# Optimization experiments

Measured on AMD Instinct MI355X. Metric: run time of the kernel, lower is better.

Reference implementation:

```python
import jax, jax.numpy as jnp
import numpy as np

B, C, H, W = 16, 512, 48, 48
INTER = 64  # C // reduction


def setup_inputs() -> dict:
    key = jax.random.key(0)
    k1, k2, k3, k4, k5 = jax.random.split(key, 5)
    s = 0.05
    return {
        "x": jax.random.normal(k1, (B, C, H, W), dtype=jnp.float32),
        "Wq": jax.random.normal(k2, (INTER, C), dtype=jnp.float32) * s,
        "Wk": jax.random.normal(k3, (INTER, C), dtype=jnp.float32) * s,
        "Wv": jax.random.normal(k4, (C, C), dtype=jnp.float32) * s,
        "gamma": jax.random.normal(k5, (1,), dtype=jnp.float32),
    }


def reference(x, Wq, Wk, Wv, gamma):
    b, c, h, w = x.shape
    n = h * w
    xf = x.reshape(b, c, n)                       # (B, C, N)
    # 1x1 convs == channel-mixing GEMMs
    q = jnp.einsum("ic,bcn->bin", Wq, xf)         # (B, inter, N)
    k = jnp.einsum("ic,bcn->bin", Wk, xf)         # (B, inter, N)
    v = jnp.einsum("oc,bcn->bon", Wv, xf)         # (B, C, N)
    # attn[b, n, m] = q[b, :, n] . k[b, :, m]; softmax over m
    attn = jnp.einsum("bin,bim->bnm", q, k)       # (B, N, N)
    attn = jax.nn.softmax(attn, axis=-1)
    # out[b, c, n] = sum_m v[b, c, m] * attn[b, n, m]
    out = jnp.einsum("bcm,bnm->bcn", v, attn).reshape(b, c, h, w)
    return gamma[0] * out + x
```

## Files before the change

kernel.cpp:

```cpp
#include <hip/hip_runtime.h>

#define BATCH 16
#define CHN   512
#define INTER 64
#define NPIX  2304

typedef _Float16 f16;
typedef _Float16 f16x8 __attribute__((ext_vector_type(8)));
typedef _Float16 f16x4 __attribute__((ext_vector_type(4)));
typedef short    s16x8 __attribute__((ext_vector_type(8)));
typedef float    f32x16 __attribute__((ext_vector_type(16)));

#define XT_OFF   ((size_t)0)
#define QT_OFF   ((size_t)37748736)
#define KT_OFF   ((size_t)42467328)
#define VB_OFF   ((size_t)47185920)
#define WHQ_OFF  ((size_t)84934656)
#define WHK_OFF  ((size_t)85000192)
#define WHV_OFF  ((size_t)85065728)

#define LOG2E 1.4426950408889634f

__device__ inline unsigned short f2bf(float f) {
    unsigned int u = __float_as_uint(f);
    unsigned int r = (u + 0x7FFFu + ((u >> 16) & 1u)) >> 16;
    return (unsigned short)r;
}

__device__ inline unsigned pack_bf16(float a, float b) {
    unsigned ua = __float_as_uint(a) + 0x8000u;
    unsigned ub = __float_as_uint(b) + 0x8000u;
    return __builtin_amdgcn_perm(ub, ua, 0x07060302u);
}

__device__ inline unsigned pack_f16(float a, float b) {
    f16 ha = (f16)a, hb = (f16)b;
    unsigned short ua = *(unsigned short*)&ha, ub = *(unsigned short*)&hb;
    return (unsigned)ua | ((unsigned)ub << 16);
}

__device__ inline float exp2_fast(float x) {
#if __has_builtin(__builtin_amdgcn_exp2f)
    return __builtin_amdgcn_exp2f(x);
#else
    float r; asm("v_exp_f32 %0, %1" : "=v"(r) : "v"(x)); return r;
#endif
}

__device__ inline void gload_lds16(const void* g, void* l) {
    __builtin_amdgcn_global_load_lds(
        (const __attribute__((address_space(1))) void*)g,
        (__attribute__((address_space(3))) void*)l, 16, 0, 0);
}

__device__ inline void swap32(unsigned x, unsigned y, unsigned& nx, unsigned& ny, int lh) {
#if __has_builtin(__builtin_amdgcn_permlane32_swap)
    auto r = __builtin_amdgcn_permlane32_swap(x, y, false, false);
    nx = r[0]; ny = r[1];
#else
    const unsigned xs = (unsigned)__shfl_xor((int)x, 32, 64);
    const unsigned ys = (unsigned)__shfl_xor((int)y, 32, 64);
    nx = lh ? ys : x;
    ny = lh ? y  : xs;
#endif
}

__global__ __launch_bounds__(256) void convert_x_kernel(
    const float* __restrict__ x, f16* __restrict__ xT)
{
    const int n0 = blockIdx.x * 64;
    const int c0 = blockIdx.y * 64;
    const int b  = blockIdx.z;
    const int t  = threadIdx.x;

    __shared__ float tile[64][65];

    {
        const int cr   = t >> 2;
        const int ncol = (t & 3) * 16;
        const float* src = x + ((size_t)b * CHN + (size_t)(c0 + cr)) * NPIX + n0 + ncol;
        #pragma unroll
        for (int u = 0; u < 4; ++u) {
            const float4 v4 = *(const float4*)(src + u * 4);
            tile[cr][ncol + u * 4 + 0] = v4.x;
            tile[cr][ncol + u * 4 + 1] = v4.y;
            tile[cr][ncol + u * 4 + 2] = v4.z;
            tile[cr][ncol + u * 4 + 3] = v4.w;
        }
    }
    __syncthreads();
    #pragma unroll
    for (int r = 0; r < 2; ++r) {
        const int id = t + r * 256;
        const int n  = id >> 3;
        const int cg = id & 7;
        f16x8 o;
        #pragma unroll
        for (int j = 0; j < 8; ++j) o[j] = (f16)tile[cg * 8 + j][n];
        *(f16x8*)(xT + ((size_t)b * NPIX + (size_t)(n0 + n)) * CHN + c0 + cg * 8) = o;
    }
}

__global__ __launch_bounds__(256) void convert_w_kernel(
    const float* __restrict__ Wq, const float* __restrict__ Wk,
    const float* __restrict__ Wv, f16* __restrict__ whq,
    f16* __restrict__ whk, f16* __restrict__ whv)
{
    const int which = blockIdx.y;
    const float* src; f16* dst; int count;
    if (which == 0)      { src = Wq; dst = whq; count = 64 * 512; }
    else if (which == 1) { src = Wk; dst = whk; count = 64 * 512; }
    else                 { src = Wv; dst = whv; count = 512 * 512; }
    const int i = (blockIdx.x * 256 + threadIdx.x) * 4;
    if (i < count) {
        const float4 v4 = *(const float4*)(src + i);
        f16x4 o;
        o[0] = (f16)v4.x; o[1] = (f16)v4.y; o[2] = (f16)v4.z; o[3] = (f16)v4.w;
        *(f16x4*)(dst + i) = o;
    }
}

__global__ __launch_bounds__(256, 2) void proj_kernel(
    const f16* __restrict__ xT, const f16* __restrict__ whq,
    const f16* __restrict__ whk, const f16* __restrict__ whv,
    f16* __restrict__ qTo, f16* __restrict__ kTo,
    unsigned short* __restrict__ vout)
{
    const int nt = blockIdx.x;
    const int rt = blockIdx.y;
    const int b  = blockIdx.z;
    const int t  = threadIdx.x;
    const int wave = t >> 6, lane = t & 63;
    const int row = lane & 31, lh = lane >> 5;

    __shared__ f16 smem[2 * 128 * 72];
    f16 (*wsm)[72] = (f16(*)[72])smem;
    f16 (*xs)[72]  = (f16(*)[72])(smem + 128 * 72);

    f32x16 acc[4];
    #pragma unroll
    for (int s = 0; s < 4; ++s)
        #pragma unroll
        for (int r = 0; r < 16; ++r) acc[s][r] = 0.0f;

    for (int c0 = 0; c0 < CHN; c0 += 64) {
        __syncthreads();
        #pragma unroll
        for (int r = 0; r < 4; ++r) {
            const int id = t + r * 256;
            const int co = id >> 3, cg = id & 7;
            const f16* src;
            if (rt == 0) src = (co < 64) ? (whq + (size_t)co * CHN)
                                         : (whk + (size_t)(co - 64) * CHN);
            else         src = whv + (size_t)((rt - 1) * 128 + co) * CHN;
            *(f16x8*)&wsm[co][cg * 8] = *(const f16x8*)(src + c0 + cg * 8);
        }
        #pragma unroll
        for (int r = 0; r < 4; ++r) {
            const int id = t + r * 256;
            const int n = id >> 3, cg = id & 7;
            *(f16x8*)&xs[n][cg * 8] =
                *(const f16x8*)(xT + ((size_t)b * NPIX + (size_t)(nt * 128 + n)) * CHN + c0 + cg * 8);
        }
        __syncthreads();

        #pragma unroll
        for (int kk = 0; kk < 64; kk += 16) {
            const f16x8 bf = *(const f16x8*)&xs[wave * 32 + row][kk + lh * 8];
            #pragma unroll
            for (int cs = 0; cs < 4; ++cs) {
                const f16x8 af = *(const f16x8*)&wsm[cs * 32 + row][kk + lh * 8];
                acc[cs] = __builtin_amdgcn_mfma_f32_32x32x16_f16(af, bf, acc[cs], 0, 0, 0);
            }
        }
    }

    __syncthreads();
    unsigned short* eb = (unsigned short*)smem;
    const int nl = wave * 32 + row;

    if (rt == 0) {
        #pragma unroll
        for (int cs = 0; cs < 4; ++cs) {
            const float sc = (cs < 2) ? LOG2E : 1.0f;
            #pragma unroll
            for (int tp = 0; tp < 8; ++tp) {
                const int r = tp * 2;
                const int i = cs * 32 + (r & 3) + 8 * (r >> 2) + 4 * lh;
                *(unsigned*)&eb[nl * 130 + i] =
                    pack_f16(acc[cs][r] * sc, acc[cs][r + 1] * sc);
            }
        }
    } else {
        #pragma unroll
        for (int cs = 0; cs < 4; ++cs)
            #pragma unroll
            for (int r = 0; r < 16; ++r) {
                const int cl = cs * 32 + (r & 3) + 8 * (r >> 2) + 4 * lh;
                eb[cl * 130 + nl] = f2bf(acc[cs][r]);
            }
    }
    __syncthreads();

    #pragma unroll
    for (int u = 0; u < 8; ++u) {
        const int id = t + u * 256;
        const int rr = id >> 4;
        const int ch = id & 15;
        const unsigned short* src = &eb[rr * 130 + ch * 8];
        s16x8 w;
        #pragma unroll
        for (int k = 0; k < 4; ++k)
            ((unsigned*)&w)[k] = *(const unsigned*)(src + k * 2);
        if (rt == 0) {
            f16* dst = (ch < 8)
                ? (qTo + ((size_t)b * NPIX + nt * 128 + rr) * INTER + ch * 8)
                : (kTo + ((size_t)b * NPIX + nt * 128 + rr) * INTER + (ch - 8) * 8);
            *(s16x8*)dst = w;
        } else {
            *(s16x8*)(vout + ((size_t)b * CHN + (size_t)((rt - 1) * 128 + rr)) * NPIX
                      + nt * 128 + ch * 8) = w;
        }
    }
}

__global__ __launch_bounds__(256, 3) void attn_kernel(
    const float* __restrict__ x, const float* __restrict__ gamma,
    const f16* __restrict__ qT, const f16* __restrict__ kT,
    const unsigned short* __restrict__ vglob, float* __restrict__ out)
{
    const int nt = blockIdx.x;
    const int cq = blockIdx.y;
    const int b  = blockIdx.z;
    const int t  = threadIdx.x;
    const int wave = t >> 6, lane = t & 63;
    const int row = lane & 31, lh = lane >> 5;

    __shared__ short vbuf[2][128 * 64];
    __shared__ f16   kbuf[2][64 * 64];

    const unsigned short* vq = vglob + ((size_t)b * CHN + (size_t)cq * 128) * NPIX;
    const f16* kb = kT + (size_t)b * NPIX * INTER;

    const int lrow = lane >> 3;
    const int lch  = lane & 7;

    const int xorv = row & 7;

    f16x8 qf[4];
    {
        const f16* qrow = qT + ((size_t)b * NPIX
                          + (size_t)(nt * 128 + wave * 32 + row)) * INTER + lh * 8;
        #pragma unroll
        for (int k0 = 0; k0 < 4; ++k0) qf[k0] = *(const f16x8*)(qrow + k0 * 16);
    }

    #pragma unroll
    for (int j = 0; j < 4; ++j) {
        const int r = j * 32 + wave * 8 + lrow;
        gload_lds16(vq + (size_t)r * NPIX + ((lch ^ (r & 7)) * 8),
                    &vbuf[0][(j * 32 + wave * 8) * 64]);
    }
    #pragma unroll
    for (int j = 0; j < 2; ++j) {
        const int r = j * 32 + wave * 8 + lrow;
        gload_lds16(kb + (size_t)r * INTER + ((lch ^ (r & 7)) * 8),
                    &kbuf[0][(j * 32 + wave * 8) * 64]);
    }
    __syncthreads();

    f32x16 accv[4];
    #pragma unroll
    for (int s = 0; s < 4; ++s)
        #pragma unroll
        for (int r = 0; r < 16; ++r) accv[s][r] = 0.0f;

    float lrun = 0.0f;
    union PB { unsigned u[4]; s16x8 v; };

    for (int it = 0; it < NPIX / 64; ++it) {
        const int cur = it & 1, nxt = cur ^ 1;
        const int m1 = (it < NPIX / 64 - 1) ? (it + 1) * 64 : 0;

        #pragma unroll
        for (int j = 0; j < 4; ++j) {
            const int r = j * 32 + wave * 8 + lrow;
            gload_lds16(vq + (size_t)r * NPIX + m1 + ((lch ^ (r & 7)) * 8),
                        &vbuf[nxt][(j * 32 + wave * 8) * 64]);
        }
        #pragma unroll
        for (int j = 0; j < 2; ++j) {
            const int r = j * 32 + wave * 8 + lrow;
            gload_lds16(kb + (size_t)(m1 + r) * INTER + ((lch ^ (r & 7)) * 8),
                        &kbuf[nxt][(j * 32 + wave * 8) * 64]);
        }

        union PB pb[4];
        #pragma unroll
        for (int mh = 0; mh < 2; ++mh) {
            f32x16 sacc;
            #pragma unroll
            for (int r = 0; r < 16; ++r) sacc[r] = 0.0f;
            #pragma unroll
            for (int k0 = 0; k0 < 4; ++k0) {
                const f16x8 af = *(const f16x8*)&kbuf[cur][(mh * 32 + row) * 64
                                    + (((k0 * 2 + lh) ^ xorv) * 8)];
                sacc = __builtin_amdgcn_mfma_f32_32x32x16_f16(af, qf[k0], sacc, 0, 0, 0);
            }
            float lp = 0.0f;
            unsigned pg[8];
            #pragma unroll
            for (int tt = 0; tt < 8; ++tt) {
                const float p0 = exp2_fast(sacc[2 * tt + 0]);
                const float p1 = exp2_fast(sacc[2 * tt + 1]);
                lp += p0 + p1;
                pg[tt] = pack_bf16(p0, p1);
            }
            lrun += lp;
            #pragma unroll
            for (int half = 0; half < 2; ++half)
                #pragma unroll
                for (int p = 0; p < 2; ++p) {
                    unsigned nx, ny;
                    swap32(pg[half * 4 + p], pg[half * 4 + 2 + p], nx, ny, lh);
                    pb[2 * mh + half].u[p]     = nx;
                    pb[2 * mh + half].u[p + 2] = ny;
                }
        }

        #pragma unroll
        for (int cs = 0; cs < 4; ++cs)
            #pragma unroll
            for (int kk = 0; kk < 4; ++kk) {
                const s16x8 va = *(const s16x8*)&vbuf[cur][(cs * 32 + row) * 64
                                    + (((kk * 2 + lh) ^ xorv) * 8)];
                accv[cs] = __builtin_amdgcn_mfma_f32_32x32x16_bf16(
                    va, pb[kk].v, accv[cs], 0, 0, 0);
            }

        __syncthreads();
    }

    const float g = gamma[0];
    const float linv = 1.0f / (lrun + __shfl_xor(lrun, 32, 64));
    const int n = nt * 128 + wave * 32 + row;

    #pragma unroll
    for (int cs = 0; cs < 4; ++cs)
        #pragma unroll
        for (int r = 0; r < 16; ++r) {
            const int c = cq * 128 + cs * 32 + (r & 3) + 8 * (r >> 2) + 4 * lh;
            const size_t idx = ((size_t)b * CHN + c) * NPIX + n;
            out[idx] = g * accv[cs][r] * linv + x[idx];
        }
}

extern "C" void kernel_launch(void* const* d_in, const int* in_sizes, int n_in,
                              void* d_out, int out_size, void* d_ws, size_t ws_size,
                              hipStream_t stream) {
    (void)in_sizes; (void)n_in; (void)out_size; (void)ws_size;
    const float* x     = (const float*)d_in[0];
    const float* Wq    = (const float*)d_in[1];
    const float* Wk    = (const float*)d_in[2];
    const float* Wv    = (const float*)d_in[3];
    const float* gamma = (const float*)d_in[4];
    float* out = (float*)d_out;
    char* ws = (char*)d_ws;

    f16* xT  = (f16*)(ws + XT_OFF);
    f16* qTp = (f16*)(ws + QT_OFF);
    f16* kTp = (f16*)(ws + KT_OFF);
    unsigned short* vb = (unsigned short*)(ws + VB_OFF);
    f16* whq = (f16*)(ws + WHQ_OFF);
    f16* whk = (f16*)(ws + WHK_OFF);
    f16* whv = (f16*)(ws + WHV_OFF);

    convert_x_kernel<<<dim3(36, 8, 16), 256, 0, stream>>>(x, xT);
    convert_w_kernel<<<dim3(256, 3, 1), 256, 0, stream>>>(Wq, Wk, Wv, whq, whk, whv);
    proj_kernel<<<dim3(18, 5, 16), 256, 0, stream>>>(xT, whq, whk, whv, qTp, kTp, vb);
    attn_kernel<<<dim3(18, 4, 16), 256, 0, stream>>>(x, gamma, qTp, kTp, vb, out);
}
```

Measured before the change: 370.4 us.

## Triple-buffer V/K LDS tiles with two-ahead prefetch and partial vmcnt waits

Replaces the double-buffered V/K shared-memory pipeline with a three-stage ring that prefetches two tiles ahead. The per-iteration __syncthreads becomes an explicit s_waitcnt vmcnt(6) plus s_barrier, so the most recent tile's loads can stay in flight across the barrier. This hides more global-load latency. It raises LDS use from 48KB to 72KB per block and lowers launch bounds from 3 to 2 blocks per CU, trading occupancy for deeper prefetch.

```diff
diff --git a/kernel.cpp b/kernel.cpp
--- a/kernel.cpp
+++ b/kernel.cpp
@@ -224,7 +224,7 @@
     }
 }
 
-__global__ __launch_bounds__(256, 3) void attn_kernel(
+__global__ __launch_bounds__(256, 2) void attn_kernel(
     const float* __restrict__ x, const float* __restrict__ gamma,
     const f16* __restrict__ qT, const f16* __restrict__ kT,
     const unsigned short* __restrict__ vglob, float* __restrict__ out)
@@ -236,8 +236,8 @@
     const int wave = t >> 6, lane = t & 63;
     const int row = lane & 31, lh = lane >> 5;
 
-    __shared__ short vbuf[2][128 * 64];
-    __shared__ f16   kbuf[2][64 * 64];
+    __shared__ short vbuf[3][128 * 64];
+    __shared__ f16   kbuf[3][64 * 64];
 
     const unsigned short* vq = vglob + ((size_t)b * CHN + (size_t)cq * 128) * NPIX;
     const f16* kb = kT + (size_t)b * NPIX * INTER;
@@ -267,7 +267,19 @@
         gload_lds16(kb + (size_t)r * INTER + ((lch ^ (r & 7)) * 8),
                     &kbuf[0][(j * 32 + wave * 8) * 64]);
     }
-    __syncthreads();
+    #pragma unroll
+    for (int j = 0; j < 4; ++j) {
+        const int r = j * 32 + wave * 8 + lrow;
+        gload_lds16(vq + (size_t)r * NPIX + 64 + ((lch ^ (r & 7)) * 8),
+                    &vbuf[1][(j * 32 + wave * 8) * 64]);
+    }
+    #pragma unroll
+    for (int j = 0; j < 2; ++j) {
+        const int r = j * 32 + wave * 8 + lrow;
+        gload_lds16(kb + (size_t)(64 + r) * INTER + ((lch ^ (r & 7)) * 8),
+                    &kbuf[1][(j * 32 + wave * 8) * 64]);
+    }
+    asm volatile("s_waitcnt vmcnt(6)\n\ts_barrier" ::: "memory");
 
     f32x16 accv[4];
     #pragma unroll
@@ -278,21 +290,26 @@
     float lrun = 0.0f;
     union PB { unsigned u[4]; s16x8 v; };
 
+    int cur = 0, nx2 = 2;
     for (int it = 0; it < NPIX / 64; ++it) {
-        const int cur = it & 1, nxt = cur ^ 1;
-        const int m1 = (it < NPIX / 64 - 1) ? (it + 1) * 64 : 0;
+        const int m2 = (it + 2 < NPIX / 64) ? (it + 2) * 64 : 0;
+
+        short* vb_s = &vbuf[0][0] + nx2 * (128 * 64);
+        f16*   kb_s = &kbuf[0][0] + nx2 * (64 * 64);
+        const short* vb_c = &vbuf[0][0] + cur * (128 * 64);
+        const f16*   kb_c = &kbuf[0][0] + cur * (64 * 64);
 
         #pragma unroll
         for (int j = 0; j < 4; ++j) {
             const int r = j * 32 + wave * 8 + lrow;
-            gload_lds16(vq + (size_t)r * NPIX + m1 + ((lch ^ (r & 7)) * 8),
-                        &vbuf[nxt][(j * 32 + wave * 8) * 64]);
+            gload_lds16(vq + (size_t)r * NPIX + m2 + ((lch ^ (r & 7)) * 8),
+                        vb_s + (j * 32 + wave * 8) * 64);
         }
         #pragma unroll
         for (int j = 0; j < 2; ++j) {
             const int r = j * 32 + wave * 8 + lrow;
-            gload_lds16(kb + (size_t)(m1 + r) * INTER + ((lch ^ (r & 7)) * 8),
-                        &kbuf[nxt][(j * 32 + wave * 8) * 64]);
+            gload_lds16(kb + (size_t)(m2 + r) * INTER + ((lch ^ (r & 7)) * 8),
+                        kb_s + (j * 32 + wave * 8) * 64);
         }
 
         union PB pb[4];
@@ -303,7 +320,7 @@
             for (int r = 0; r < 16; ++r) sacc[r] = 0.0f;
             #pragma unroll
             for (int k0 = 0; k0 < 4; ++k0) {
-                const f16x8 af = *(const f16x8*)&kbuf[cur][(mh * 32 + row) * 64
+                const f16x8 af = *(const f16x8*)&kb_c[(mh * 32 + row) * 64
                                     + (((k0 * 2 + lh) ^ xorv) * 8)];
                 sacc = __builtin_amdgcn_mfma_f32_32x32x16_f16(af, qf[k0], sacc, 0, 0, 0);
             }
@@ -332,14 +349,19 @@
         for (int cs = 0; cs < 4; ++cs)
             #pragma unroll
             for (int kk = 0; kk < 4; ++kk) {
-                const s16x8 va = *(const s16x8*)&vbuf[cur][(cs * 32 + row) * 64
+                const s16x8 va = *(const s16x8*)&vb_c[(cs * 32 + row) * 64
                                     + (((kk * 2 + lh) ^ xorv) * 8)];
                 accv[cs] = __builtin_amdgcn_mfma_f32_32x32x16_bf16(
                     va, pb[kk].v, accv[cs], 0, 0, 0);
             }
 
-        __syncthreads();
-    }
+        asm volatile("s_waitcnt vmcnt(6)\n\ts_barrier" ::: "memory");
+
+        cur = (cur == 2) ? 0 : cur + 1;
+        nx2 = (nx2 == 2) ? 0 : nx2 + 1;
+    }
+
+    asm volatile("s_waitcnt vmcnt(0)" ::: "memory");
 
     const float g = gamma[0];
     const float linv = 1.0f / (lrun + __shfl_xor(lrun, 32, 64));
```

Measured after the change: 368.0 us. No clear change (-0.6%).
